# Kernel tuning notes

Hardware: AMD Instinct MI355X
Metric: run time of the kernel (lower is better)

The kernel has to match this reference:

```python
import jax, jax.numpy as jnp
import numpy as np

C_IN = 64
C_H = 128
K = 5  # filter_size
EPS = 1e-5


def _conv1x1(w, x):
    # w: [O, I], x: [B, I, H, W]
    return jnp.einsum('oi,bihw->bohw', w, x)


def _conv3x3(w, x):
    # w: [O, I, 3, 3], x: [B, I, H, W], SAME padding
    return jax.lax.conv_general_dilated(
        x, w, window_strides=(1, 1), padding='SAME',
        dimension_numbers=('NCHW', 'OIHW', 'NCHW'))


def _layernorm_c(x, g, b):
    # LayerNorm over the channel dim (original permutes to NHWC, norms last dim)
    m = jnp.mean(x, axis=1, keepdims=True)
    v = jnp.mean(jnp.square(x - m), axis=1, keepdims=True)
    xn = (x - m) * jax.lax.rsqrt(v + EPS)
    return xn * g[None, :, None, None] + b[None, :, None, None]


def _dynamic_filter(x, w_df1, w_df2):
    # 3x3 conv -> ReLU -> 1x1 conv producing C_H*K*K channels
    h = jax.nn.relu(_conv3x3(w_df1, x))
    return _conv1x1(w_df2, h)


def _apply_dynamic_filter(feat, filt):
    # feat: [B, C, H, W]; filt: [B, C*K*K, H, W]
    # Equivalent to unfold(K, pad=K//2) * filt summed over the K*K taps,
    # but computed as K*K shifted multiply-accumulates (no huge intermediate).
    B, C, H, W = feat.shape
    filt = filt.reshape(B, C, K * K, H, W)
    p = K // 2
    fp = jnp.pad(feat, ((0, 0), (0, 0), (p, p), (p, p)))
    out = jnp.zeros_like(feat)
    k = 0
    for ki in range(K):
        for kj in range(K):
            out = out + fp[:, :, ki:ki + H, kj:kj + W] * filt[:, :, k]
            k += 1
    return out


def setup_inputs() -> dict:
    key = jax.random.key(0)
    ks = jax.random.split(key, 8)
    B, H, W = 2, 128, 128
    s = 0.05
    return {
        'rgb_high': jax.random.normal(ks[0], (B, C_IN, H, W), jnp.float32),
        'event': jax.random.normal(ks[1], (B, C_IN, H, W), jnp.float32),
        'w_in': jax.random.normal(ks[2], (C_H, C_IN), jnp.float32) * s,
        'ln_g': jnp.ones((C_H,), jnp.float32),
        'ln_b': jnp.zeros((C_H,), jnp.float32),
        'w_df1': jax.random.normal(ks[3], (C_H, C_H, 3, 3), jnp.float32) * s,
        'w_df2': jax.random.normal(ks[4], (C_H * K * K, C_H), jnp.float32) * s,
        'w_sp': jax.random.normal(ks[5], (C_H, C_H), jnp.float32) * s,
        'w_out': jax.random.normal(ks[6], (C_IN, C_H), jnp.float32) * s,
    }


def reference(rgb_high, event, w_in, ln_g, ln_b, w_df1, w_df2, w_sp, w_out):
    rgb_feat = _layernorm_c(_conv1x1(w_in, rgb_high), ln_g, ln_b)
    event_feat = _layernorm_c(_conv1x1(w_in, event), ln_g, ln_b)
    rgb_filter = _dynamic_filter(rgb_feat, w_df1, w_df2)
    event_filter = _dynamic_filter(event_feat, w_df1, w_df2)
    rgb_enh = _apply_dynamic_filter(rgb_feat, rgb_filter)
    event_enh = _apply_dynamic_filter(event_feat, event_filter)
    rgb_filtered = rgb_enh * jax.nn.sigmoid(_conv1x1(w_sp, event_enh))
    rgb_fused = rgb_enh + rgb_filtered + rgb_feat
    rgb_norm = _layernorm_c(rgb_fused, ln_g, ln_b)
    return _conv1x1(w_out, rgb_norm)
```

## Files before the change

### kernel.cpp

```cpp
#include <hip/hip_runtime.h>
#include <math.h>

#define BLK 256

typedef unsigned short ushort;
typedef unsigned int uint;
typedef __attribute__((ext_vector_type(8))) short short8;
typedef __attribute__((ext_vector_type(4))) float f32x4;

constexpr int C_Hc = 128;
constexpr int C_INc = 64;
constexpr int Hh = 128;
constexpr int Ww = 128;
constexpr int HWc = Hh * Ww;
constexpr int Bb = 2;
constexpr float EPSV = 1e-5f;

__device__ __forceinline__ float bf2f(ushort u) {
    union { uint u32; float f; } v; v.u32 = (uint)u << 16; return v.f;
}
__device__ __forceinline__ ushort f2bf(float x) {
    union { float f; uint u; } v; v.f = x;
    uint r = (v.u + 0x7FFFu + ((v.u >> 16) & 1u)) >> 16;
    return (ushort)r;
}
__device__ __forceinline__ uint pack2(float a, float b) {
    return (uint)f2bf(a) | ((uint)f2bf(b) << 16);
}
__device__ __forceinline__ void gload16(const ushort* g, ushort* l) {
    __builtin_amdgcn_global_load_lds(
        (const __attribute__((address_space(1))) void*)g,
        (__attribute__((address_space(3))) void*)l, 16, 0, 0);
}

__global__ __launch_bounds__(BLK) void k_prep(
    const float* __restrict__ w1, const float* __restrict__ w2,
    const float* __restrict__ wsp,
    ushort* __restrict__ wA, ushort* __restrict__ w2b,
    ushort* __restrict__ wspb)
{
    int idx = blockIdx.x * BLK + threadIdx.x;
    if (idx < 147456) {
        int tap = idx >> 14, r = idx & 16383;
        int chunk = r >> 10, co = (r >> 3) & 127, e = r & 7;
        int ci = chunk * 8 + e;
        wA[idx] = f2bf(w1[(co * 128 + ci) * 9 + tap]);
    } else if (idx < 557056) {
        int o = idx - 147456;
        int k = o >> 14, r = o & 16383;
        int chunk = r >> 10, co = (r >> 3) & 127, e = r & 7;
        int ci = chunk * 8 + e;
        w2b[o] = f2bf(w2[(co * 25 + k) * 128 + ci]);
    } else if (idx < 573440) {
        int o = idx - 557056;
        int chunk = o >> 10, co = (o >> 3) & 127, e = o & 7;
        wspb[o] = f2bf(wsp[co * 128 + chunk * 8 + e]);
    }
}

__global__ __launch_bounds__(BLK) void k_in_ln(
    const float* __restrict__ xr, const float* __restrict__ xe,
    const float* __restrict__ w_in, const float* __restrict__ lng,
    const float* __restrict__ lnb,
    ushort* __restrict__ fTr, ushort* __restrict__ fTe,
    float* __restrict__ featrT)
{
    int bid  = blockIdx.x;
    int simg = bid >> 9;
    int rem  = bid & 511;
    int b    = rem >> 8;
    int base = (rem & 255) * 64;
    const float* x = simg ? xe : xr;
    ushort* fT = simg ? fTe : fTr;
    int tid  = threadIdx.x;
    int lane = tid & 63;
    int cg   = tid >> 6;

    __shared__ float xs[C_INc][64];
    __shared__ float r1[4][64], r2[4][64];
    __shared__ ushort lb[64][136];
    __shared__ float  lf[64][132];

    #pragma unroll
    for (int r = 0; r < 16; ++r) {
        int i = cg * 16 + r;
        xs[i][lane] = x[(b * C_INc + i) * HWc + base + lane];
    }
    __syncthreads();

    float acc[32];
    #pragma unroll
    for (int cc = 0; cc < 32; ++cc) acc[cc] = 0.f;

    for (int i4 = 0; i4 < 16; ++i4) {
        float x0 = xs[i4 * 4 + 0][lane];
        float x1 = xs[i4 * 4 + 1][lane];
        float x2 = xs[i4 * 4 + 2][lane];
        float x3 = xs[i4 * 4 + 3][lane];
        #pragma unroll
        for (int cc = 0; cc < 32; ++cc) {
            float4 wv = *reinterpret_cast<const float4*>(
                &w_in[(cg * 32 + cc) * C_INc + i4 * 4]);
            acc[cc] += wv.x * x0 + wv.y * x1 + wv.z * x2 + wv.w * x3;
        }
    }

    float s1 = 0.f, s2 = 0.f;
    #pragma unroll
    for (int cc = 0; cc < 32; ++cc) { s1 += acc[cc]; s2 += acc[cc] * acc[cc]; }
    r1[cg][lane] = s1; r2[cg][lane] = s2;
    __syncthreads();
    float m   = (r1[0][lane] + r1[1][lane] + r1[2][lane] + r1[3][lane]) * (1.f / C_Hc);
    float ex2 = (r2[0][lane] + r2[1][lane] + r2[2][lane] + r2[3][lane]) * (1.f / C_Hc);
    float rs  = rsqrtf(ex2 - m * m + EPSV);

    #pragma unroll
    for (int cc = 0; cc < 32; cc += 4) {
        int c0 = cg * 32 + cc;
        float4 g4 = *reinterpret_cast<const float4*>(&lng[c0]);
        float4 b4 = *reinterpret_cast<const float4*>(&lnb[c0]);
        float4 y;
        y.x = (acc[cc + 0] - m) * rs * g4.x + b4.x;
        y.y = (acc[cc + 1] - m) * rs * g4.y + b4.y;
        y.z = (acc[cc + 2] - m) * rs * g4.z + b4.z;
        y.w = (acc[cc + 3] - m) * rs * g4.w + b4.w;
        *reinterpret_cast<uint*>(&lb[lane][c0])     = pack2(y.x, y.y);
        *reinterpret_cast<uint*>(&lb[lane][c0 + 2]) = pack2(y.z, y.w);
        if (!simg)
            *reinterpret_cast<float4*>(&lf[lane][c0]) = y;
    }
    __syncthreads();

    long long tb = ((long long)((b << 14) + base)) << 7;
    #pragma unroll
    for (int t = 0; t < 4; ++t) {
        int j  = tid + (t << 8);
        int px = j >> 4;
        int w0 = (j & 15) << 3;
        uint4 v = *reinterpret_cast<const uint4*>(&lb[px][w0]);
        *reinterpret_cast<uint4*>(&fT[tb + ((long long)px << 7) + w0]) = v;
    }
    if (!simg) {
        #pragma unroll
        for (int t = 0; t < 8; ++t) {
            int j  = tid + (t << 8);
            int px = j >> 5;
            int w0 = (j & 31) << 2;
            float4 v = *reinterpret_cast<const float4*>(&lf[px][w0]);
            *reinterpret_cast<float4*>(&featrT[tb + ((long long)px << 7) + w0]) = v;
        }
    }
}

__global__ __launch_bounds__(BLK, 3) void k_conv3(
    const ushort* __restrict__ fTr, const ushort* __restrict__ fTe,
    const ushort* __restrict__ wA,
    ushort* __restrict__ hTr, ushort* __restrict__ hTe)
{
    int bid = blockIdx.x;
    int ph = bid & 1, h0 = (bid >> 1) & 127, b = (bid >> 8) & 1, s = bid >> 9;
    int w0 = ph << 6;
    const ushort* fT = s ? fTe : fTr;
    ushort* hT = s ? hTe : hTr;
    int tid = threadIdx.x, lane = tid & 63, wv = tid >> 6;
    int lpx = lane & 15, lk = lane >> 4;
    int co0 = wv * 32;

    __shared__ ushort ft[16 * 198 * 8];

    const long long ibase = (long long)(b << 14);

    for (int i = tid; i < 16 * 198; i += BLK) {
        int chunk = i / 198;
        int rem = i - chunk * 198;
        int row = rem / 66, col = rem - row * 66;
        int gh = h0 + row - 1, gw = w0 + col - 1;
        uint4 v = make_uint4(0, 0, 0, 0);
        if ((unsigned)gh < 128u && (unsigned)gw < 128u)
            v = *reinterpret_cast<const uint4*>(
                &fT[((ibase + (gh << 7) + gw) << 7) + (chunk << 3)]);
        *reinterpret_cast<uint4*>(&ft[i << 3]) = v;
    }
    __syncthreads();

    f32x4 acc[2][4];
    #pragma unroll
    for (int f = 0; f < 2; ++f)
        #pragma unroll
        for (int p = 0; p < 4; ++p) acc[f][p] = f32x4{0.f, 0.f, 0.f, 0.f};

    for (int tap = 0; tap < 9; ++tap) {
        int ki = tap / 3, kj = tap - ki * 3;
        const ushort* wtp = &wA[tap << 14];
        short8 a[2][4];
        #pragma unroll
        for (int f = 0; f < 2; ++f) {
            int co = co0 + f * 16 + lpx;
            #pragma unroll
            for (int q = 0; q < 4; ++q)
                a[f][q] = *reinterpret_cast<const short8*>(
                    &wtp[(((q * 4 + lk) << 7) + co) << 3]);
        }
        #pragma unroll
        for (int p = 0; p < 4; ++p) {
            int col = p * 16 + lpx + kj;
            short8 bq[4];
            #pragma unroll
            for (int q = 0; q < 4; ++q)
                bq[q] = *reinterpret_cast<const short8*>(
                    &ft[((q * 4 + lk) * 198 + ki * 66 + col) << 3]);
            #pragma unroll
            for (int f = 0; f < 2; ++f)
                #pragma unroll
                for (int q = 0; q < 4; ++q)
                    acc[f][p] = __builtin_amdgcn_mfma_f32_16x16x32_bf16(
                        a[f][q], bq[q], acc[f][p], 0, 0, 0);
        }
    }

    long long obase = (ibase + ((long long)h0 << 7)) << 7;
    #pragma unroll
    for (int f = 0; f < 2; ++f)
        #pragma unroll
        for (int p = 0; p < 4; ++p) {
            int c  = co0 + f * 16 + (lk << 2);
            int px = w0 + p * 16 + lpx;
            float v0 = fmaxf(acc[f][p][0], 0.f), v1 = fmaxf(acc[f][p][1], 0.f);
            float v2 = fmaxf(acc[f][p][2], 0.f), v3 = fmaxf(acc[f][p][3], 0.f);
            ushort* dst = &hT[obase + ((long long)px << 7) + c];
            *reinterpret_cast<uint*>(&dst[0]) = pack2(v0, v1);
            *reinterpret_cast<uint*>(&dst[2]) = pack2(v2, v3);
        }
}

__global__ __launch_bounds__(512, 2) void k_dfapply(
    const ushort* __restrict__ hTr, const ushort* __restrict__ hTe,
    const ushort* __restrict__ fTr, const ushort* __restrict__ fTe,
    const ushort* __restrict__ w2b,
    ushort* __restrict__ enhr, ushort* __restrict__ enhe)
{
    int bid = blockIdx.x;
    int s = bid >> 7, b = (bid >> 6) & 1, hp = bid & 63;
    int h0g = hp << 1;
    const ushort* hT = s ? hTe : hTr;
    const ushort* fT = s ? fTe : fTr;
    ushort* enh = s ? enhe : enhr;
    int tid = threadIdx.x, lane = tid & 63, wv = tid >> 6;
    int lpx = lane & 15, lk = lane >> 4;
    int r    = wv >> 2;
    int co0  = (wv & 1) * 64, px0 = ((wv >> 1) & 1) * 64;
    int h0   = h0g + r;

    __shared__ ushort wk[2][16 * 128 * 8];
    __shared__ ushort fr[2][128 * 16 * 8];

    const long long ibase = (long long)(b << 14);
    const long long rowbase = (ibase + ((long long)h0 << 7)) << 7;

    short8 bq[4][4];
    #pragma unroll
    for (int p = 0; p < 4; ++p) {
        int px = px0 + p * 16 + lpx;
        #pragma unroll
        for (int q = 0; q < 4; ++q)
            bq[p][q] = *reinterpret_cast<const short8*>(
                &hT[rowbase + ((long long)px << 7) + ((q * 4 + lk) << 3)]);
    }

    auto stage_rows = [&](int dh) {
        for (int rr = 0; rr < 2; ++rr) {
            int gh = h0g + rr + dh;
            if ((unsigned)gh < 128u) {
                const ushort* rowsrc = fT + ((ibase + ((long long)gh << 7)) << 7);
                #pragma unroll
                for (int t = 0; t < 4; ++t) {
                    int j = tid + (t << 9);
                    int px = j >> 4, u = j & 15;
                    int su = u ^ (px & 15);
                    gload16(&rowsrc[(px << 7) + (su << 3)], &fr[rr][j << 3]);
                }
            }
        }
    };

    #pragma unroll
    for (int t = 0; t < 4; ++t) {
        int j = tid + (t << 9);
        gload16(&w2b[j << 3], &wk[0][j << 3]);
    }
    stage_rows(-2);
    __syncthreads();

    f32x4 osum[4][4];
    #pragma unroll
    for (int f = 0; f < 4; ++f)
        #pragma unroll
        for (int p = 0; p < 4; ++p) osum[f][p] = f32x4{0.f, 0.f, 0.f, 0.f};

    for (int k = 0; k < 25; ++k) {
        int cur = k & 1;
        if (k < 24) {
            const ushort* srcb = &w2b[(k + 1) << 14];
            #pragma unroll
            for (int t = 0; t < 4; ++t) {
                int j = tid + (t << 9);
                gload16(&srcb[j << 3], &wk[cur ^ 1][j << 3]);
            }
        }
        int k5 = k / 5;
        int dh = k5 - 2, dw = k - k5 * 5 - 2;
        int gh = h0 + dh;
        bool rowok = (unsigned)gh < 128u;

        uint2 featv[4][4];
        #pragma unroll
        for (int p = 0; p < 4; ++p) {
            int gw = px0 + p * 16 + lpx + dw;
            bool ok = rowok && ((unsigned)gw < 128u);
            #pragma unroll
            for (int f = 0; f < 4; ++f) {
                int c4 = co0 + f * 16 + (lk << 2);
                uint2 v = make_uint2(0, 0);
                if (ok) v = *reinterpret_cast<const uint2*>(
                    &fr[r][(((gw << 4) + ((c4 >> 3) ^ (gw & 15))) << 3)
                           + (c4 & 7)]);
                featv[p][f] = v;
            }
        }

        #pragma unroll
        for (int f = 0; f < 4; ++f) {
            int co = co0 + f * 16 + lpx;
            short8 a[4];
            #pragma unroll
            for (int q = 0; q < 4; ++q)
                a[q] = *reinterpret_cast<const short8*>(
                    &wk[cur][(((q * 4 + lk) << 7) + co) << 3]);
            __builtin_amdgcn_s_setprio(1);
            #pragma unroll
            for (int p = 0; p < 4; ++p) {
                f32x4 fac = f32x4{0.f, 0.f, 0.f, 0.f};
                #pragma unroll
                for (int q = 0; q < 4; ++q)
                    fac = __builtin_amdgcn_mfma_f32_16x16x32_bf16(
                        a[q], bq[p][q], fac, 0, 0, 0);
                uint2 fv = featv[p][f];
                osum[f][p][0] += fac[0] * bf2f((ushort)(fv.x & 0xffff));
                osum[f][p][1] += fac[1] * bf2f((ushort)(fv.x >> 16));
                osum[f][p][2] += fac[2] * bf2f((ushort)(fv.y & 0xffff));
                osum[f][p][3] += fac[3] * bf2f((ushort)(fv.y >> 16));
            }
            __builtin_amdgcn_s_setprio(0);
        }
        __syncthreads();
        if ((k % 5 == 4) && k < 24) {
            stage_rows(k / 5 - 1);
            __syncthreads();
        }
    }

    #pragma unroll
    for (int f = 0; f < 4; ++f)
        #pragma unroll
        for (int p = 0; p < 4; ++p) {
            int c  = co0 + f * 16 + (lk << 2);
            int px = px0 + p * 16 + lpx;
            int slot = (c >> 3) ^ (px & 15);
            uint2 o;
            o.x = pack2(osum[f][p][0], osum[f][p][1]);
            o.y = pack2(osum[f][p][2], osum[f][p][3]);
            *reinterpret_cast<uint2*>(
                &fr[r][(((px << 4) + slot) << 3) + (c & 7)]) = o;
        }
    __syncthreads();

    #pragma unroll
    for (int t = 0; t < 8; ++t) {
        int j  = tid + (t << 9);
        int rr = j >> 11;
        int jj = j & 2047;
        int px = jj >> 4, u = jj & 15;
        int chunk = u ^ (px & 15);
        uint4 v = *reinterpret_cast<const uint4*>(&fr[rr][jj << 3]);
        *reinterpret_cast<uint4*>(
            &enh[((ibase + ((long long)(h0g + rr) << 7)) << 7)
                 + ((long long)px << 7) + (chunk << 3)]) = v;
    }
}

__global__ __launch_bounds__(BLK, 2) void k_final(
    const ushort* __restrict__ enhr, const ushort* __restrict__ enhe,
    const float* __restrict__ featrT,
    const ushort* __restrict__ wspb, const float* __restrict__ w_out,
    const float* __restrict__ lng, const float* __restrict__ lnb,
    float* __restrict__ out)
{
    int bid = blockIdx.x;
    int b = bid >> 8;
    int px0g = (bid & 255) * 64;
    int tid = threadIdx.x, lane = tid & 63, wv = tid >> 6;
    int lpx = lane & 15, lk = lane >> 4;

    __shared__ float woA[4096];
    __shared__ float woB[4096];
    __shared__ float xs[128][64];
    __shared__ float p1[4][64], p2[4][64];
    ushort* es = (ushort*)woA;

    const long long ebase = ((long long)((b << 14) + px0g)) << 7;

    #pragma unroll
    for (int t = 0; t < 4; ++t) {
        int j = tid + (t << 8);
        int chunk = j >> 6, px = j & 63;
        *reinterpret_cast<uint4*>(&es[j << 3]) =
            *reinterpret_cast<const uint4*>(
                &enhe[ebase + ((long long)px << 7) + (chunk << 3)]);
    }
    __syncthreads();

    int co0 = wv * 32;
    f32x4 sp[2][4];
    #pragma unroll
    for (int f = 0; f < 2; ++f)
        #pragma unroll
        for (int p = 0; p < 4; ++p) sp[f][p] = f32x4{0.f, 0.f, 0.f, 0.f};
    #pragma unroll
    for (int q = 0; q < 4; ++q) {
        short8 a[2], bb[4];
        #pragma unroll
        for (int f = 0; f < 2; ++f)
            a[f] = *reinterpret_cast<const short8*>(
                &wspb[((((q * 4 + lk) << 7) + co0 + f * 16 + lpx)) << 3]);
        #pragma unroll
        for (int p = 0; p < 4; ++p)
            bb[p] = *reinterpret_cast<const short8*>(
                &es[((((q * 4 + lk) << 6) + p * 16 + lpx)) << 3]);
        #pragma unroll
        for (int f = 0; f < 2; ++f)
            #pragma unroll
            for (int p = 0; p < 4; ++p)
                sp[f][p] = __builtin_amdgcn_mfma_f32_16x16x32_bf16(
                    a[f], bb[p], sp[f][p], 0, 0, 0);
    }

    float fu[2][4][4];
    float s1[4] = {0.f, 0.f, 0.f, 0.f}, s2[4] = {0.f, 0.f, 0.f, 0.f};
    #pragma unroll
    for (int f = 0; f < 2; ++f) {
        int c4 = co0 + f * 16 + (lk << 2);
        #pragma unroll
        for (int p = 0; p < 4; ++p) {
            int px = p * 16 + lpx;
            long long poff = ebase + ((long long)px << 7) + c4;
            uint2 re2 = *reinterpret_cast<const uint2*>(&enhr[poff]);
            float4 rf4 = *reinterpret_cast<const float4*>(&featrT[poff]);
            float re[4] = { bf2f((ushort)(re2.x & 0xffff)), bf2f((ushort)(re2.x >> 16)),
                            bf2f((ushort)(re2.y & 0xffff)), bf2f((ushort)(re2.y >> 16)) };
            float rf[4] = { rf4.x, rf4.y, rf4.z, rf4.w };
            #pragma unroll
            for (int rr = 0; rr < 4; ++rr) {
                float sg = 1.f / (1.f + __expf(-sp[f][p][rr]));
                float v = re[rr] * (1.f + sg) + rf[rr];
                fu[f][p][rr] = v;
                s1[p] += v; s2[p] += v * v;
            }
        }
    }
    #pragma unroll
    for (int p = 0; p < 4; ++p) {
        s1[p] += __shfl_xor(s1[p], 16); s1[p] += __shfl_xor(s1[p], 32);
        s2[p] += __shfl_xor(s2[p], 16); s2[p] += __shfl_xor(s2[p], 32);
    }
    if (lk == 0) {
        #pragma unroll
        for (int p = 0; p < 4; ++p) {
            p1[wv][p * 16 + lpx] = s1[p];
            p2[wv][p * 16 + lpx] = s2[p];
        }
    }
    __syncthreads();

    #pragma unroll
    for (int i = 0; i < 8; ++i) {
        int fidx = tid + (i << 8);
        float4 v = *reinterpret_cast<const float4*>(&w_out[fidx << 2]);
        if (fidx < 1024) reinterpret_cast<float4*>(woA)[fidx] = v;
        else             reinterpret_cast<float4*>(woB)[fidx - 1024] = v;
    }

    float mm[4], rs[4];
    #pragma unroll
    for (int p = 0; p < 4; ++p) {
        int px = p * 16 + lpx;
        float m   = (p1[0][px] + p1[1][px] + p1[2][px] + p1[3][px]) * (1.f / 128.f);
        float ex2 = (p2[0][px] + p2[1][px] + p2[2][px] + p2[3][px]) * (1.f / 128.f);
        mm[p] = m;
        rs[p] = rsqrtf(ex2 - m * m + EPSV);
    }

    #pragma unroll
    for (int f = 0; f < 2; ++f) {
        int c4 = co0 + f * 16 + (lk << 2);
        float4 g = *reinterpret_cast<const float4*>(&lng[c4]);
        float4 bta = *reinterpret_cast<const float4*>(&lnb[c4]);
        #pragma unroll
        for (int p = 0; p < 4; ++p) {
            int px = p * 16 + lpx;
            xs[c4 + 0][px] = (fu[f][p][0] - mm[p]) * rs[p] * g.x + bta.x;
            xs[c4 + 1][px] = (fu[f][p][1] - mm[p]) * rs[p] * g.y + bta.y;
            xs[c4 + 2][px] = (fu[f][p][2] - mm[p]) * rs[p] * g.z + bta.z;
            xs[c4 + 3][px] = (fu[f][p][3] - mm[p]) * rs[p] * g.w + bta.w;
        }
    }
    __syncthreads();

    int co0o = wv * 16;
    const float* wop = (wv & 2) ? woB : woA;
    int wbase = (wv & 1) << 11;
    float oacc[16];
    #pragma unroll
    for (int oo = 0; oo < 16; ++oo) oacc[oo] = 0.f;
    for (int j4 = 0; j4 < 32; ++j4) {
        float x0 = xs[j4 * 4 + 0][lane];
        float x1 = xs[j4 * 4 + 1][lane];
        float x2 = xs[j4 * 4 + 2][lane];
        float x3 = xs[j4 * 4 + 3][lane];
        #pragma unroll
        for (int oo = 0; oo < 16; ++oo) {
            float4 wv4 = *reinterpret_cast<const float4*>(
                &wop[wbase + oo * C_Hc + j4 * 4]);
            oacc[oo] += wv4.x * x0 + wv4.y * x1 + wv4.z * x2 + wv4.w * x3;
        }
    }
    #pragma unroll
    for (int oo = 0; oo < 16; ++oo)
        out[((long long)(b * C_INc + co0o + oo) << 14) + px0g + lane] = oacc[oo];
}

extern "C" void kernel_launch(void* const* d_in, const int* in_sizes, int n_in,
                              void* d_out, int out_size, void* d_ws, size_t ws_size,
                              hipStream_t stream)
{
    const float* rgb  = (const float*)d_in[0];
    const float* evt  = (const float*)d_in[1];
    const float* w_in = (const float*)d_in[2];
    const float* lng  = (const float*)d_in[3];
    const float* lnb  = (const float*)d_in[4];
    const float* w1   = (const float*)d_in[5];
    const float* w2   = (const float*)d_in[6];
    const float* wsp  = (const float*)d_in[7];
    const float* wout = (const float*)d_in[8];
    float* out = (float*)d_out;

    float* ws = (float*)d_ws;
    ushort* fTr    = (ushort*)(ws);
    ushort* fTe    = (ushort*)(ws + 2097152);
    ushort* hTr    = (ushort*)(ws + 4194304);
    ushort* hTe    = (ushort*)(ws + 6291456);
    ushort* enhr   = (ushort*)(ws + 8388608);
    ushort* enhe   = (ushort*)(ws + 10485760);
    float*  featrT = (float*)(ws + 12582912);
    ushort* wA     = (ushort*)(ws + 16777216);
    ushort* w2b    = (ushort*)(ws + 16850944);
    ushort* wspb   = (ushort*)(ws + 17055744);

    k_prep<<<2240, BLK, 0, stream>>>(w1, w2, wsp, wA, w2b, wspb);
    k_in_ln<<<2 * Bb * 256, BLK, 0, stream>>>(rgb, evt, w_in, lng, lnb,
                                              fTr, fTe, featrT);
    k_conv3<<<1024, BLK, 0, stream>>>(fTr, fTe, wA, hTr, hTe);
    k_dfapply<<<256, 512, 0, stream>>>(hTr, hTe, fTr, fTe, w2b, enhr, enhe);
    k_final<<<Bb * 256, BLK, 0, stream>>>(enhr, enhe, featrT, wspb, wout,
                                          lng, lnb, out);
}
```

Before: 200.0 us.

## Split dynamic-filter apply to one row per block, single-buffer weights for occupancy

k_dfapply now assigns one image row per 512-thread block instead of two, doubling the grid to 512 blocks, with each wave covering 32 pixels instead of 64. Weight and feature LDS buffers drop from double to single, and the next tap's weight load is issued after the barrier rather than overlapped with compute. Launch bounds rise to 4 blocks per CU to use the smaller LDS and register footprint. This trades load/compute overlap and weight reuse per block for more parallelism and occupancy, and the filter weights are now fetched twice as often overall.

```diff
diff --git a/kernel.cpp b/kernel.cpp
--- a/kernel.cpp
+++ b/kernel.cpp
@@ -233,33 +233,30 @@
         }
 }
 
-__global__ __launch_bounds__(512, 2) void k_dfapply(
+__global__ __launch_bounds__(512, 4) void k_dfapply(
     const ushort* __restrict__ hTr, const ushort* __restrict__ hTe,
     const ushort* __restrict__ fTr, const ushort* __restrict__ fTe,
     const ushort* __restrict__ w2b,
     ushort* __restrict__ enhr, ushort* __restrict__ enhe)
 {
     int bid = blockIdx.x;
-    int s = bid >> 7, b = (bid >> 6) & 1, hp = bid & 63;
-    int h0g = hp << 1;
+    int s = bid >> 8, b = (bid >> 7) & 1, h0 = bid & 127;
     const ushort* hT = s ? hTe : hTr;
     const ushort* fT = s ? fTe : fTr;
     ushort* enh = s ? enhe : enhr;
     int tid = threadIdx.x, lane = tid & 63, wv = tid >> 6;
     int lpx = lane & 15, lk = lane >> 4;
-    int r    = wv >> 2;
-    int co0  = (wv & 1) * 64, px0 = ((wv >> 1) & 1) * 64;
-    int h0   = h0g + r;
-
-    __shared__ ushort wk[2][16 * 128 * 8];
-    __shared__ ushort fr[2][128 * 16 * 8];
+    int co0 = (wv & 1) * 64, px0 = (wv >> 1) * 32;
+
+    __shared__ ushort wk[16 * 128 * 8];
+    __shared__ ushort fr[128 * 16 * 8];
 
     const long long ibase = (long long)(b << 14);
     const long long rowbase = (ibase + ((long long)h0 << 7)) << 7;
 
-    short8 bq[4][4];
-    #pragma unroll
-    for (int p = 0; p < 4; ++p) {
+    short8 bq[2][4];
+    #pragma unroll
+    for (int p = 0; p < 2; ++p) {
         int px = px0 + p * 16 + lpx;
         #pragma unroll
         for (int q = 0; q < 4; ++q)
@@ -267,18 +264,16 @@
                 &hT[rowbase + ((long long)px << 7) + ((q * 4 + lk) << 3)]);
     }
 
-    auto stage_rows = [&](int dh) {
-        for (int rr = 0; rr < 2; ++rr) {
-            int gh = h0g + rr + dh;
-            if ((unsigned)gh < 128u) {
-                const ushort* rowsrc = fT + ((ibase + ((long long)gh << 7)) << 7);
-                #pragma unroll
-                for (int t = 0; t < 4; ++t) {
-                    int j = tid + (t << 9);
-                    int px = j >> 4, u = j & 15;
-                    int su = u ^ (px & 15);
-                    gload16(&rowsrc[(px << 7) + (su << 3)], &fr[rr][j << 3]);
-                }
+    auto stage_row = [&](int dh) {
+        int gh = h0 + dh;
+        if ((unsigned)gh < 128u) {
+            const ushort* rowsrc = fT + ((ibase + ((long long)gh << 7)) << 7);
+            #pragma unroll
+            for (int t = 0; t < 4; ++t) {
+                int j = tid + (t << 9);
+                int px = j >> 4, u = j & 15;
+                int su = u ^ (px & 15);
+                gload16(&rowsrc[(px << 7) + (su << 3)], &fr[j << 3]);
             }
         }
     };
@@ -286,35 +281,26 @@
     #pragma unroll
     for (int t = 0; t < 4; ++t) {
         int j = tid + (t << 9);
-        gload16(&w2b[j << 3], &wk[0][j << 3]);
-    }
-    stage_rows(-2);
-    __syncthreads();
-
-    f32x4 osum[4][4];
+        gload16(&w2b[j << 3], &wk[j << 3]);
+    }
+    stage_row(-2);
+    __syncthreads();
+
+    f32x4 osum[4][2];
     #pragma unroll
     for (int f = 0; f < 4; ++f)
         #pragma unroll
-        for (int p = 0; p < 4; ++p) osum[f][p] = f32x4{0.f, 0.f, 0.f, 0.f};
+        for (int p = 0; p < 2; ++p) osum[f][p] = f32x4{0.f, 0.f, 0.f, 0.f};
 
     for (int k = 0; k < 25; ++k) {
-        int cur = k & 1;
-        if (k < 24) {
-            const ushort* srcb = &w2b[(k + 1) << 14];
-            #pragma unroll
-            for (int t = 0; t < 4; ++t) {
-                int j = tid + (t << 9);
-                gload16(&srcb[j << 3], &wk[cur ^ 1][j << 3]);
-            }
-        }
         int k5 = k / 5;
         int dh = k5 - 2, dw = k - k5 * 5 - 2;
         int gh = h0 + dh;
         bool rowok = (unsigned)gh < 128u;
 
-        uint2 featv[4][4];
-        #pragma unroll
-        for (int p = 0; p < 4; ++p) {
+        uint2 featv[2][4];
+        #pragma unroll
+        for (int p = 0; p < 2; ++p) {
             int gw = px0 + p * 16 + lpx + dw;
             bool ok = rowok && ((unsigned)gw < 128u);
             #pragma unroll
@@ -322,8 +308,8 @@
                 int c4 = co0 + f * 16 + (lk << 2);
                 uint2 v = make_uint2(0, 0);
                 if (ok) v = *reinterpret_cast<const uint2*>(
-                    &fr[r][(((gw << 4) + ((c4 >> 3) ^ (gw & 15))) << 3)
-                           + (c4 & 7)]);
+                    &fr[(((gw << 4) + ((c4 >> 3) ^ (gw & 15))) << 3)
+                        + (c4 & 7)]);
                 featv[p][f] = v;
             }
         }
@@ -335,10 +321,10 @@
             #pragma unroll
             for (int q = 0; q < 4; ++q)
                 a[q] = *reinterpret_cast<const short8*>(
-                    &wk[cur][(((q * 4 + lk) << 7) + co) << 3]);
+                    &wk[(((q * 4 + lk) << 7) + co) << 3]);
             __builtin_amdgcn_s_setprio(1);
             #pragma unroll
-            for (int p = 0; p < 4; ++p) {
+            for (int p = 0; p < 2; ++p) {
                 f32x4 fac = f32x4{0.f, 0.f, 0.f, 0.f};
                 #pragma unroll
                 for (int q = 0; q < 4; ++q)
@@ -353,8 +339,15 @@
             __builtin_amdgcn_s_setprio(0);
         }
         __syncthreads();
-        if ((k % 5 == 4) && k < 24) {
-            stage_rows(k / 5 - 1);
+        if (k < 24) {
+            const ushort* srcb = &w2b[(k + 1) << 14];
+            #pragma unroll
+            for (int t = 0; t < 4; ++t) {
+                int j = tid + (t << 9);
+                gload16(&srcb[j << 3], &wk[j << 3]);
+            }
+            if (k - k5 * 5 == 4)
+                stage_row(k5 - 1);
             __syncthreads();
         }
     }
@@ -362,7 +355,7 @@
     #pragma unroll
     for (int f = 0; f < 4; ++f)
         #pragma unroll
-        for (int p = 0; p < 4; ++p) {
+        for (int p = 0; p < 2; ++p) {
             int c  = co0 + f * 16 + (lk << 2);
             int px = px0 + p * 16 + lpx;
             int slot = (c >> 3) ^ (px & 15);
@@ -370,21 +363,18 @@
             o.x = pack2(osum[f][p][0], osum[f][p][1]);
             o.y = pack2(osum[f][p][2], osum[f][p][3]);
             *reinterpret_cast<uint2*>(
-                &fr[r][(((px << 4) + slot) << 3) + (c & 7)]) = o;
-        }
-    __syncthreads();
-
-    #pragma unroll
-    for (int t = 0; t < 8; ++t) {
+                &fr[(((px << 4) + slot) << 3) + (c & 7)]) = o;
+        }
+    __syncthreads();
+
+    #pragma unroll
+    for (int t = 0; t < 4; ++t) {
         int j  = tid + (t << 9);
-        int rr = j >> 11;
-        int jj = j & 2047;
-        int px = jj >> 4, u = jj & 15;
+        int px = j >> 4, u = j & 15;
         int chunk = u ^ (px & 15);
-        uint4 v = *reinterpret_cast<const uint4*>(&fr[rr][jj << 3]);
+        uint4 v = *reinterpret_cast<const uint4*>(&fr[j << 3]);
         *reinterpret_cast<uint4*>(
-            &enh[((ibase + ((long long)(h0g + rr) << 7)) << 7)
-                 + ((long long)px << 7) + (chunk << 3)]) = v;
+            &enh[rowbase + ((long long)px << 7) + (chunk << 3)]) = v;
     }
 }
 
@@ -569,7 +559,7 @@
     k_in_ln<<<2 * Bb * 256, BLK, 0, stream>>>(rgb, evt, w_in, lng, lnb,
                                               fTr, fTe, featrT);
     k_conv3<<<1024, BLK, 0, stream>>>(fTr, fTe, wA, hTr, hTe);
-    k_dfapply<<<256, 512, 0, stream>>>(hTr, hTe, fTr, fTe, w2b, enhr, enhe);
+    k_dfapply<<<512, 512, 0, stream>>>(hTr, hTe, fTr, fTe, w2b, enhr, enhe);
     k_final<<<Bb * 256, BLK, 0, stream>>>(enhr, enhe, featrT, wspb, wout,
                                           lng, lnb, out);
 }
```

Measured after the change: 311.6 us. 1.56x slower.
